# Optimization experiments

Hardware: AMD Instinct MI355X
Metric: run time of the kernel (lower is better)

Reference implementation:

```python
import jax, jax.numpy as jnp
import numpy as np
from jax import lax

D_MODEL = 1024
D_STATE = 16
D_CONV = 4
EXPAND = 2
D_INNER = EXPAND * D_MODEL  # 2048
DT_RANK = (D_MODEL + 15) // 16  # 64 (ceil(d_model/16), mamba default)
BATCH = 2
SEQLEN = 1024


def setup_inputs() -> dict:
    key = jax.random.key(0)
    ks = jax.random.split(key, 12)
    s = lambda k, shape, sc=0.02: jax.random.normal(k, shape, jnp.float32) * sc
    # A init: S4D-real, A_log = log(1..d_state) tiled over channels
    A_log = jnp.log(jnp.tile(jnp.arange(1, D_STATE + 1, dtype=jnp.float32), (D_INNER, 1)))
    # dt bias init so softplus(dt_bias) ~ 0.01
    dt_bias = jnp.log(jnp.expm1(jnp.full((D_INNER,), 0.01, jnp.float32)))
    return {
        "x": jax.random.normal(ks[0], (BATCH, SEQLEN, D_MODEL), jnp.float32),
        "in_proj_w": s(ks[1], (2 * D_INNER, D_MODEL)),
        "conv_w": s(ks[2], (D_INNER, 1, D_CONV), 0.1),
        "conv_b": s(ks[3], (D_INNER,), 0.1),
        "x_proj_w": s(ks[4], (DT_RANK + 2 * D_STATE, D_INNER)),
        "dt_proj_w": s(ks[5], (D_INNER, DT_RANK), 0.1),
        "dt_proj_b": dt_bias,
        "A_log": A_log,
        "D": jnp.ones((D_INNER,), jnp.float32),
        "out_proj_w": s(ks[6], (D_MODEL, D_INNER)),
        "ln1_g": jnp.ones((D_MODEL,), jnp.float32),
        "ln1_b": jnp.zeros((D_MODEL,), jnp.float32),
        "ln2_g": jnp.ones((D_MODEL,), jnp.float32),
        "ln2_b": jnp.zeros((D_MODEL,), jnp.float32),
        "ffn_w1": s(ks[7], (4 * D_MODEL, D_MODEL)),
        "ffn_b1": jnp.zeros((4 * D_MODEL,), jnp.float32),
        "ffn_w2": s(ks[8], (D_MODEL, 4 * D_MODEL)),
        "ffn_b2": jnp.zeros((D_MODEL,), jnp.float32),
    }


def _layernorm(x, g, b, eps=1e-5):
    mu = jnp.mean(x, axis=-1, keepdims=True)
    var = jnp.mean(jnp.square(x - mu), axis=-1, keepdims=True)
    return (x - mu) * lax.rsqrt(var + eps) * g + b


def _mamba(x, in_proj_w, conv_w, conv_b, x_proj_w, dt_proj_w, dt_proj_b,
           A_log, D, out_proj_w):
    Bsz, L, _ = x.shape
    xz = x @ in_proj_w.T                       # [B, L, 2*d_inner]
    xi, z = jnp.split(xz, 2, axis=-1)          # each [B, L, d_inner]
    # causal depthwise conv1d over time
    xc = xi.transpose(0, 2, 1)                 # [B, d_inner, L]
    xc = lax.conv_general_dilated(
        xc, conv_w, window_strides=(1,), padding=[(D_CONV - 1, 0)],
        feature_group_count=D_INNER,
        dimension_numbers=("NCH", "OIH", "NCH"))
    xc = xc + conv_b[None, :, None]
    xc = jax.nn.silu(xc).transpose(0, 2, 1)    # [B, L, d_inner]
    # input-dependent SSM params
    x_dbl = xc @ x_proj_w.T                    # [B, L, dt_rank + 2*d_state]
    dt, Bmat, Cmat = jnp.split(x_dbl, [DT_RANK, DT_RANK + D_STATE], axis=-1)
    dt = jax.nn.softplus(dt @ dt_proj_w.T + dt_proj_b)   # [B, L, d_inner]
    A = -jnp.exp(A_log)                        # [d_inner, d_state]
    dA = jnp.exp(dt[..., None] * A)                       # [B, L, d_inner, d_state]
    dBx = dt[..., None] * Bmat[:, :, None, :] * xc[..., None]  # [B, L, d_inner, d_state]
    # selective scan over time
    def step(h, inp):
        dA_t, dBx_t, C_t = inp
        h = dA_t * h + dBx_t                   # [B, d_inner, d_state]
        y = jnp.einsum("bdn,bn->bd", h, C_t)
        return h, y
    h0 = jnp.zeros((Bsz, D_INNER, D_STATE), x.dtype)
    _, ys = lax.scan(step, h0,
                     (dA.transpose(1, 0, 2, 3),
                      dBx.transpose(1, 0, 2, 3),
                      Cmat.transpose(1, 0, 2)))
    y = ys.transpose(1, 0, 2)                  # [B, L, d_inner]
    y = y + D * xc
    y = y * jax.nn.silu(z)
    return y @ out_proj_w.T                    # [B, L, d_model]


def reference(x, in_proj_w, conv_w, conv_b, x_proj_w, dt_proj_w, dt_proj_b,
              A_log, D, out_proj_w, ln1_g, ln1_b, ln2_g, ln2_b,
              ffn_w1, ffn_b1, ffn_w2, ffn_b2):
    # x = x + Mamba(LN1(x))
    x = x + _mamba(_layernorm(x, ln1_g, ln1_b), in_proj_w, conv_w, conv_b,
                   x_proj_w, dt_proj_w, dt_proj_b, A_log, D, out_proj_w)
    # x = x + FFN(LN2(x))  (dropout inactive in eval)
    h = _layernorm(x, ln2_g, ln2_b)
    f = jax.nn.relu(h @ ffn_w1.T + ffn_b1) @ ffn_w2.T + ffn_b2
    return x + f
```

## Files before the change

### kernel.cpp

```cpp
#include <hip/hip_runtime.h>
#include <hip/hip_bf16.h>

#define T_TOK 2048
#define LSEQ  1024
#define DM    1024
#define DI    2048
#define LDW2  72

using bf16 = __hip_bfloat16;
typedef __attribute__((ext_vector_type(8))) short short8;
typedef __attribute__((ext_vector_type(4))) short short4b;
typedef __attribute__((ext_vector_type(4))) float floatx4;

__device__ inline float to_f(float v) { return v; }
__device__ inline float to_f(bf16 v) { return __bfloat162float(v); }
__device__ inline bf16  f2bf(float v) { return __float2bfloat16(v); }
__device__ inline float bf2f(short s) { return __bfloat162float(__builtin_bit_cast(bf16, s)); }

__device__ inline short8 ld8(const bf16* p) { return *(const short8*)p; }
__device__ inline short8 ld8(const float* p) {
    floatx4 f0 = *(const floatx4*)p;
    floatx4 f1 = *(const floatx4*)(p + 4);
    short8 r;
#pragma unroll
    for (int i = 0; i < 4; ++i) {
        r[i]     = __builtin_bit_cast(short, __float2bfloat16(f0[i]));
        r[i + 4] = __builtin_bit_cast(short, __float2bfloat16(f1[i]));
    }
    return r;
}

__device__ __forceinline__ void gload16(const void* g, void* l) {
    __builtin_amdgcn_global_load_lds(
        (const __attribute__((address_space(1))) unsigned int*)g,
        (__attribute__((address_space(3))) unsigned int*)l, 16, 0, 0);
}

__device__ __forceinline__ int swz64(int row, int col) {
    return row * 64 + (col ^ ((row & 7) << 3));
}

template<int EPI, int KS>
__device__ __forceinline__ void gemm_core(
    const bf16* __restrict__ A, int lda,
    const bf16* __restrict__ W, int K,
    float* __restrict__ outF, bf16* __restrict__ outB, int ldc,
    const float* __restrict__ bias, size_t zstr)
{
    __shared__ __align__(16) bf16 sA[128 * 64];
    __shared__ __align__(16) bf16 sW[128 * 64];
    const int tid  = threadIdx.x;
    const int lane = tid & 63, wid = tid >> 6;

    const int nwg = gridDim.x * gridDim.y * gridDim.z;
    const int lin = blockIdx.x + gridDim.x * (blockIdx.y + gridDim.y * blockIdx.z);
    const int sid = (lin & 7) * (nwg >> 3) + (lin >> 3);
    const int bx  = sid % gridDim.x;
    const int byz = sid / gridDim.x;
    const int by  = byz % gridDim.y;
    const int bz  = byz / gridDim.y;

    const int m0 = bx * 128, n0 = by * 128;
    const int wm = (wid >> 2) * 64;
    const int wn = (wid & 3) * 32;
    const int lr = lane & 15, lh = lane >> 4;

    const int r0  = tid >> 3;
    const int gc0 = ((tid & 7) * 8) ^ ((r0 & 7) << 3);

    const int kBeg = bz * (K / KS);
    const int kEnd = kBeg + K / KS;

    const bf16* Ag0 = A + (size_t)(m0 + r0)      * lda + kBeg + gc0;
    const bf16* Ag1 = A + (size_t)(m0 + r0 + 64) * lda + kBeg + gc0;
    const bf16* Wg0 = W + (size_t)(n0 + r0)      * K   + kBeg + gc0;
    const bf16* Wg1 = W + (size_t)(n0 + r0 + 64) * K   + kBeg + gc0;

    bf16* sA0 = sA + wid * 512;
    bf16* sA1 = sA + 4096 + wid * 512;
    bf16* sW0 = sW + wid * 512;
    bf16* sW1 = sW + 4096 + wid * 512;

    floatx4 acc[4][2];
#pragma unroll
    for (int i = 0; i < 4; ++i)
#pragma unroll
        for (int j = 0; j < 2; ++j) acc[i][j] = (floatx4){0.f, 0.f, 0.f, 0.f};

    for (int k0 = kBeg; k0 < kEnd; k0 += 64) {
        __syncthreads();
        gload16(Ag0, sA0);
        gload16(Ag1, sA1);
        gload16(Wg0, sW0);
        gload16(Wg1, sW1);
        Ag0 += 64; Ag1 += 64; Wg0 += 64; Wg1 += 64;
        __syncthreads();

#pragma unroll
        for (int kk = 0; kk < 2; ++kk) {
            short8 af[4], wf[2];
#pragma unroll
            for (int i = 0; i < 4; ++i)
                af[i] = *(const short8*)(sA + swz64(wm + i * 16 + lr, kk * 32 + lh * 8));
#pragma unroll
            for (int j = 0; j < 2; ++j)
                wf[j] = *(const short8*)(sW + swz64(wn + j * 16 + lr, kk * 32 + lh * 8));
#pragma unroll
            for (int i = 0; i < 4; ++i)
#pragma unroll
                for (int j = 0; j < 2; ++j)
                    acc[i][j] = __builtin_amdgcn_mfma_f32_16x16x32_bf16(af[i], wf[j], acc[i][j], 0, 0, 0);
        }
    }

#pragma unroll
    for (int i = 0; i < 4; ++i) {
#pragma unroll
        for (int j = 0; j < 2; ++j) {
#pragma unroll
            for (int r = 0; r < 4; ++r) {
                int row = m0 + wm + i * 16 + lh * 4 + r;
                int col = n0 + wn + j * 16 + lr;
                size_t off = (size_t)row * ldc + col;
                float c = acc[i][j][r];
                if (EPI == 0) {
                    outB[off] = f2bf(c);
                } else if (EPI == 2) {
                    float v = c + bias[col];
                    outB[off] = f2bf((v > 15.f) ? v : log1pf(__expf(v)));
                } else if (EPI == 4) {
                    float v = c + bias[col];
                    outB[off] = f2bf(v > 0.f ? v : 0.f);
                } else if (EPI == 7) {
                    outF[off + (size_t)bz * zstr] = c;
                } else if (EPI == 8) {
                    outB[off + (size_t)bz * zstr] = f2bf(c);
                }
            }
        }
    }
}

__launch_bounds__(512, 4)
__global__ void g_inproj(const bf16* __restrict__ A, const bf16* __restrict__ W,
                         bf16* __restrict__ outB)
{ gemm_core<0, 1>(A, DM, W, DM, nullptr, outB, 4096, nullptr, 0); }

__launch_bounds__(512, 4)
__global__ void g_xproj(const bf16* __restrict__ A, const bf16* __restrict__ W,
                        float* __restrict__ outF)
{ gemm_core<7, 16>(A, DI, W, DI, outF, nullptr, 128, nullptr, (size_t)T_TOK * 128); }

__launch_bounds__(512, 4)
__global__ void g_outproj(const bf16* __restrict__ A, const bf16* __restrict__ W,
                          bf16* __restrict__ outB)
{ gemm_core<8, 4>(A, DI, W, DI, nullptr, outB, DM, nullptr, (size_t)T_TOK * DM); }

__launch_bounds__(512, 4)
__global__ void g_ffn1(const bf16* __restrict__ A, const bf16* __restrict__ W,
                       bf16* __restrict__ outB, const float* __restrict__ bias)
{ gemm_core<4, 1>(A, DM, W, DM, nullptr, outB, 4096, bias, 0); }

__launch_bounds__(512, 4)
__global__ void g_ffn2_4(const bf16* __restrict__ A, const bf16* __restrict__ W,
                         bf16* __restrict__ outB)
{ gemm_core<8, 4>(A, 4096, W, 4096, nullptr, outB, DM, nullptr, (size_t)T_TOK * DM); }

__launch_bounds__(512, 4)
__global__ void g_ffn2_2(const bf16* __restrict__ A, const bf16* __restrict__ W,
                         bf16* __restrict__ outB)
{ gemm_core<8, 2>(A, 4096, W, 4096, nullptr, outB, DM, nullptr, (size_t)T_TOK * DM); }

__launch_bounds__(256)
__global__ void cvtw(const float* __restrict__ src, bf16* __restrict__ dst)
{
    size_t i = ((size_t)blockIdx.x * 256 + threadIdx.x) * 8;
    *(short8*)(dst + i) = ld8(src + i);
}

__launch_bounds__(256)
__global__ void cvtw5(const float* __restrict__ s0, bf16* __restrict__ d0,
                      const float* __restrict__ s1, bf16* __restrict__ d1,
                      const float* __restrict__ s2, bf16* __restrict__ d2,
                      const float* __restrict__ s3, bf16* __restrict__ d3,
                      const float* __restrict__ s4, bf16* __restrict__ d4)
{
    constexpr size_t N0 = (size_t)2 * DI * DM;
    constexpr size_t N1 = (size_t)DM * DI;
    constexpr size_t N2 = (size_t)4 * DM * DM;
    constexpr size_t N3 = (size_t)DM * 4 * DM;
    size_t i = ((size_t)blockIdx.x * 256 + threadIdx.x) * 8;
    if (i < N0) { *(short8*)(d0 + i) = ld8(s0 + i); return; }
    i -= N0;
    if (i < N1) { *(short8*)(d1 + i) = ld8(s1 + i); return; }
    i -= N1;
    if (i < N2) { *(short8*)(d2 + i) = ld8(s2 + i); return; }
    i -= N2;
    if (i < N3) { *(short8*)(d3 + i) = ld8(s3 + i); return; }
    i -= N3;
    int row = (int)(i >> 11);
    if (row < 96) { *(short8*)(d4 + i) = ld8(s4 + i); }
    else { *(short8*)(d4 + i) = (short8){0,0,0,0,0,0,0,0}; }
}

__launch_bounds__(256)
__global__ void gemm_dt64(const float* __restrict__ A,
                          const float* __restrict__ W,
                          const float* __restrict__ bias,
                          bf16* __restrict__ outB)
{
    __shared__ __align__(16) bf16 sA[32 * LDW2];
    __shared__ __align__(16) bf16 sW[128 * LDW2];
    const int tid = threadIdx.x;
    const int lane = tid & 63, w = tid >> 6;
    const int m0 = blockIdx.x * 32, n0 = blockIdx.y * 128;

    {
        int ar = tid >> 3, ac = (tid & 7) * 8;
        *(short8*)(sA + ar * LDW2 + ac) = ld8(A + (size_t)(m0 + ar) * 128 + ac);
        int wr = tid >> 1, wc = (tid & 1) * 32;
        const float* wp = W + (size_t)(n0 + wr) * 64 + wc;
        *(short8*)(sW + wr * LDW2 + wc)      = ld8(wp);
        *(short8*)(sW + wr * LDW2 + wc + 8)  = ld8(wp + 8);
        *(short8*)(sW + wr * LDW2 + wc + 16) = ld8(wp + 16);
        *(short8*)(sW + wr * LDW2 + wc + 24) = ld8(wp + 24);
    }
    __syncthreads();

    const int lr = lane & 15, lh = lane >> 4;
    floatx4 acc[2][2];
#pragma unroll
    for (int i = 0; i < 2; ++i)
#pragma unroll
        for (int j = 0; j < 2; ++j) acc[i][j] = (floatx4){0.f, 0.f, 0.f, 0.f};

#pragma unroll
    for (int kk = 0; kk < 2; ++kk) {
        short8 af[2], wf[2];
#pragma unroll
        for (int i = 0; i < 2; ++i)
            af[i] = *(const short8*)(sA + (i * 16 + lr) * LDW2 + kk * 32 + lh * 8);
#pragma unroll
        for (int j = 0; j < 2; ++j)
            wf[j] = *(const short8*)(sW + (w * 32 + j * 16 + lr) * LDW2 + kk * 32 + lh * 8);
#pragma unroll
        for (int i = 0; i < 2; ++i)
#pragma unroll
            for (int j = 0; j < 2; ++j)
                acc[i][j] = __builtin_amdgcn_mfma_f32_16x16x32_bf16(af[i], wf[j], acc[i][j], 0, 0, 0);
    }

#pragma unroll
    for (int i = 0; i < 2; ++i) {
#pragma unroll
        for (int j = 0; j < 2; ++j) {
#pragma unroll
            for (int r = 0; r < 4; ++r) {
                int row = m0 + i * 16 + lh * 4 + r;
                int col = n0 + w * 32 + j * 16 + lr;
                float v = acc[i][j][r] + bias[col];
                outB[(size_t)row * DI + col] = f2bf((v > 15.f) ? v : log1pf(__expf(v)));
            }
        }
    }
}

__launch_bounds__(256)
__global__ void reduce16(const float* __restrict__ P, float* __restrict__ out)
{
    int i = blockIdx.x * 256 + threadIdx.x;
    const floatx4* P4 = (const floatx4*)P;
    floatx4 s = (floatx4){0.f, 0.f, 0.f, 0.f};
#pragma unroll
    for (int z = 0; z < 16; ++z) s += P4[(size_t)z * 65536 + i];
    ((floatx4*)out)[i] = s;
}

__launch_bounds__(256)
__global__ void red4_ln(const bf16* __restrict__ P, const float* __restrict__ x,
                        const float* __restrict__ g, const float* __restrict__ bb,
                        float* __restrict__ x2, bf16* __restrict__ h1)
{
    int t = blockIdx.x, tid = threadIdx.x;
    size_t rowoff = (size_t)t * DM + tid * 4;
    floatx4 xv = *(const floatx4*)(x + rowoff);
    float v[4];
#pragma unroll
    for (int i = 0; i < 4; ++i) v[i] = xv[i];
#pragma unroll
    for (int z = 0; z < 4; ++z) {
        short4b p = *(const short4b*)(P + (size_t)z * T_TOK * DM + rowoff);
#pragma unroll
        for (int i = 0; i < 4; ++i) v[i] += bf2f(p[i]);
    }
    *(floatx4*)(x2 + rowoff) = (floatx4){v[0], v[1], v[2], v[3]};
    float s = v[0] + v[1] + v[2] + v[3];
    float ss = v[0]*v[0] + v[1]*v[1] + v[2]*v[2] + v[3]*v[3];
#pragma unroll
    for (int o = 1; o < 64; o <<= 1) { s += __shfl_xor(s, o); ss += __shfl_xor(ss, o); }
    __shared__ float red[8];
    int lane = tid & 63, wid = tid >> 6;
    if (lane == 0) { red[wid] = s; red[wid + 4] = ss; }
    __syncthreads();
    s  = red[0] + red[1] + red[2] + red[3];
    ss = red[4] + red[5] + red[6] + red[7];
    float mu  = s * (1.f / DM);
    float var = ss * (1.f / DM) - mu * mu;
    float rs  = rsqrtf(var + 1e-5f);
    int c = tid * 4;
    short4b o4;
#pragma unroll
    for (int i = 0; i < 4; ++i)
        o4[i] = __builtin_bit_cast(short, f2bf((v[i] - mu) * rs * g[c + i] + bb[c + i]));
    *(short4b*)(h1 + rowoff) = o4;
}

template<int Z>
__launch_bounds__(256)
__global__ void red_bias_resid(const bf16* __restrict__ P, const float* __restrict__ bias,
                               const float* __restrict__ resid, float* __restrict__ out)
{
    size_t base = ((size_t)blockIdx.x * 256 + threadIdx.x) * 8;
    int c = (int)(base & (DM - 1));
    floatx4 b0 = *(const floatx4*)(bias + c);
    floatx4 b1 = *(const floatx4*)(bias + c + 4);
    floatx4 x0 = *(const floatx4*)(resid + base);
    floatx4 x1 = *(const floatx4*)(resid + base + 4);
    float s[8];
#pragma unroll
    for (int j = 0; j < 4; ++j) { s[j] = x0[j] + b0[j]; s[j + 4] = x1[j] + b1[j]; }
#pragma unroll
    for (int z = 0; z < Z; ++z) {
        short8 p = *(const short8*)(P + (size_t)z * T_TOK * DM + base);
#pragma unroll
        for (int j = 0; j < 8; ++j) s[j] += bf2f(p[j]);
    }
    *(floatx4*)(out + base)     = (floatx4){s[0], s[1], s[2], s[3]};
    *(floatx4*)(out + base + 4) = (floatx4){s[4], s[5], s[6], s[7]};
}

__launch_bounds__(256)
__global__ void ln_kernel(const float* __restrict__ x, const float* __restrict__ g,
                          const float* __restrict__ bb, bf16* __restrict__ out)
{
    int t = blockIdx.x, tid = threadIdx.x;
    const float* xr = x + (size_t)t * DM;
    float v[4], s = 0.f, ss = 0.f;
#pragma unroll
    for (int i = 0; i < 4; ++i) {
        v[i] = xr[tid + i * 256];
        s += v[i]; ss += v[i] * v[i];
    }
#pragma unroll
    for (int o = 1; o < 64; o <<= 1) { s += __shfl_xor(s, o); ss += __shfl_xor(ss, o); }
    __shared__ float red[8];
    int lane = tid & 63, wid = tid >> 6;
    if (lane == 0) { red[wid] = s; red[wid + 4] = ss; }
    __syncthreads();
    s  = red[0] + red[1] + red[2] + red[3];
    ss = red[4] + red[5] + red[6] + red[7];
    float mu  = s * (1.f / DM);
    float var = ss * (1.f / DM) - mu * mu;
    float rs  = rsqrtf(var + 1e-5f);
#pragma unroll
    for (int i = 0; i < 4; ++i) {
        int c = tid + i * 256;
        out[(size_t)t * DM + c] = f2bf((v[i] - mu) * rs * g[c] + bb[c]);
    }
}

__launch_bounds__(256)
__global__ void conv_silu(const bf16* __restrict__ xz, const float* __restrict__ cw,
                          const float* __restrict__ cb, bf16* __restrict__ xcb)
{
    int idx = (blockIdx.x * 256 + threadIdx.x) * 8;
    int d  = idx & (DI - 1);
    int tk = idx >> 11;
    int t  = tk & (LSEQ - 1);
    const short8 zero = {0, 0, 0, 0, 0, 0, 0, 0};
    short8 x3 = ld8(xz + (size_t)tk * 4096 + d);
    short8 x2 = (t >= 1) ? ld8(xz + (size_t)(tk - 1) * 4096 + d) : zero;
    short8 x1 = (t >= 2) ? ld8(xz + (size_t)(tk - 2) * 4096 + d) : zero;
    short8 x0 = (t >= 3) ? ld8(xz + (size_t)(tk - 3) * 4096 + d) : zero;
    short8 r;
#pragma unroll
    for (int j = 0; j < 8; ++j) {
        floatx4 wv = *(const floatx4*)(cw + (size_t)(d + j) * 4);
        float acc = cb[d + j]
                  + wv[0] * bf2f(x0[j]) + wv[1] * bf2f(x1[j])
                  + wv[2] * bf2f(x2[j]) + wv[3] * bf2f(x3[j]);
        float s = acc / (1.f + __expf(-acc));
        r[j] = __builtin_bit_cast(short, f2bf(s));
    }
    *(short8*)(xcb + idx) = r;
}

__launch_bounds__(256)
__global__ void padw_kernel(const float* __restrict__ w, bf16* __restrict__ wp)
{
    int idx = blockIdx.x * 256 + threadIdx.x;
    int row = idx >> 11;
    wp[idx] = (row < 96) ? f2bf(w[idx]) : f2bf(0.f);
}

template<int NCH_>
__launch_bounds__(256)
__global__ void scan_part1(const bf16* __restrict__ dt, const bf16* __restrict__ xc,
                           const float* __restrict__ xdbl, const float* __restrict__ A_log,
                           float* __restrict__ Ssum, float* __restrict__ hend)
{
    constexpr int CLEN_ = LSEQ / NCH_;
    constexpr int LOGN  = (NCH_ == 64) ? 6 : 5;
    int G = blockIdx.x * 256 + threadIdx.x;
    int half = G & 1;
    int d = (G >> 1) & (DI - 1);
    int c = (G >> 12) & (NCH_ - 1);
    int b = G >> (12 + LOGN);
    int n0 = half * 8;

    floatx4 al0 = *(const floatx4*)(A_log + d * 16 + n0);
    floatx4 al1 = *(const floatx4*)(A_log + d * 16 + n0 + 4);
    float a[8];
#pragma unroll
    for (int j = 0; j < 4; ++j) { a[j] = -__expf(al0[j]); a[j + 4] = -__expf(al1[j]); }

    const bf16*  dt_p = dt   + (size_t)b * LSEQ * DI + d;
    const bf16*  xc_p = xc   + (size_t)b * LSEQ * DI + d;
    const float* xb_p = xdbl + (size_t)b * LSEQ * 128 + 64 + n0;

    float h[8];
#pragma unroll
    for (int j = 0; j < 8; ++j) h[j] = 0.f;
    float S = 0.f;

    const int t0 = c * CLEN_;
#pragma unroll 4
    for (int t = t0; t < t0 + CLEN_; ++t) {
        float dtv = to_f(dt_p[(size_t)t * DI]);
        float xv  = to_f(xc_p[(size_t)t * DI]);
        floatx4 B0 = *(const floatx4*)(xb_p + (size_t)t * 128);
        floatx4 B1 = *(const floatx4*)(xb_p + (size_t)t * 128 + 4);
        S += dtv;
        float dx = dtv * xv;
#pragma unroll
        for (int j = 0; j < 4; ++j) {
            h[j]     = fmaf(__expf(dtv * a[j]),     h[j],     dx * B0[j]);
            h[j + 4] = fmaf(__expf(dtv * a[j + 4]), h[j + 4], dx * B1[j]);
        }
    }

    size_t cid = (size_t)(b * NCH_ + c) * DI + d;
    if (half == 0) Ssum[cid] = S;
    float* he = hend + cid * 16 + n0;
    *(floatx4*)he       = (floatx4){h[0], h[1], h[2], h[3]};
    *(floatx4*)(he + 4) = (floatx4){h[4], h[5], h[6], h[7]};
}

template<int NCH_>
__launch_bounds__(256)
__global__ void scan_prefix(const float* __restrict__ A_log, const float* __restrict__ Ssum,
                            float* __restrict__ hend)
{
    int tid = blockIdx.x * 256 + threadIdx.x;
    int n = tid & 15;
    int d = (tid >> 4) & (DI - 1);
    int b = tid >> 15;
    float a = -__expf(A_log[d * 16 + n]);

    size_t row = (size_t)b * NCH_ * DI + d;
    float Sc = Ssum[row];
    float E  = hend[row * 16 + n];
    float h = 0.f;
    for (int c = 0; c < NCH_; ++c) {
        size_t nrow = row + DI;
        float Sn = 0.f, En = 0.f;
        if (c + 1 < NCH_) { Sn = Ssum[nrow]; En = hend[nrow * 16 + n]; }
        float P = __expf(a * Sc);
        hend[row * 16 + n] = h;
        h  = fmaf(P, h, E);
        Sc = Sn; E = En; row = nrow;
    }
}

template<int NCH_>
__launch_bounds__(256)
__global__ void scan_part2(const bf16* __restrict__ dt, const bf16* __restrict__ xc,
                           const float* __restrict__ xdbl, const bf16* __restrict__ xz,
                           const float* __restrict__ hinit, const float* __restrict__ A_log,
                           const float* __restrict__ Dp, bf16* __restrict__ Y)
{
    constexpr int CLEN_ = LSEQ / NCH_;
    constexpr int LOGN  = (NCH_ == 64) ? 6 : 5;
    int G = blockIdx.x * 256 + threadIdx.x;
    int half = G & 1;
    int d = (G >> 1) & (DI - 1);
    int c = (G >> 12) & (NCH_ - 1);
    int b = G >> (12 + LOGN);
    int n0 = half * 8;

    floatx4 al0 = *(const floatx4*)(A_log + d * 16 + n0);
    floatx4 al1 = *(const floatx4*)(A_log + d * 16 + n0 + 4);
    float a[8];
#pragma unroll
    for (int j = 0; j < 4; ++j) { a[j] = -__expf(al0[j]); a[j + 4] = -__expf(al1[j]); }
    float Dd = Dp[d];

    size_t cid = (size_t)(b * NCH_ + c) * DI + d;
    const float* hi = hinit + cid * 16 + n0;
    floatx4 h0 = *(const floatx4*)hi;
    floatx4 h1 = *(const floatx4*)(hi + 4);
    float h[8] = {h0[0], h0[1], h0[2], h0[3], h1[0], h1[1], h1[2], h1[3]};

    const bf16*  dt_p = dt   + (size_t)b * LSEQ * DI + d;
    const bf16*  xc_p = xc   + (size_t)b * LSEQ * DI + d;
    const float* xb_p = xdbl + (size_t)b * LSEQ * 128 + 64 + n0;
    const float* xcc_p= xdbl + (size_t)b * LSEQ * 128 + 80 + n0;
    const bf16*  z_p  = xz   + (size_t)b * LSEQ * 4096 + DI + d;
    bf16* y_p = Y + (size_t)b * LSEQ * DI + d;

    const int t0 = c * CLEN_;
#pragma unroll 4
    for (int t = t0; t < t0 + CLEN_; ++t) {
        float dtv = to_f(dt_p[(size_t)t * DI]);
        float xv  = to_f(xc_p[(size_t)t * DI]);
        float zv  = to_f(z_p[(size_t)t * 4096]);
        floatx4 B0 = *(const floatx4*)(xb_p  + (size_t)t * 128);
        floatx4 B1 = *(const floatx4*)(xb_p  + (size_t)t * 128 + 4);
        floatx4 C0 = *(const floatx4*)(xcc_p + (size_t)t * 128);
        floatx4 C1 = *(const floatx4*)(xcc_p + (size_t)t * 128 + 4);
        float dx = dtv * xv;
        float p = 0.f;
#pragma unroll
        for (int j = 0; j < 4; ++j) {
            h[j]     = fmaf(__expf(dtv * a[j]),     h[j],     dx * B0[j]);
            p = fmaf(h[j], C0[j], p);
            h[j + 4] = fmaf(__expf(dtv * a[j + 4]), h[j + 4], dx * B1[j]);
            p = fmaf(h[j + 4], C1[j], p);
        }
        p += __shfl_xor(p, 1);
        if (half == 0) {
            float pp = p + Dd * xv;
            float sz = zv / (1.f + __expf(-zv));
            y_p[(size_t)t * DI] = f2bf(pp * sz);
        }
    }
}

extern "C" void kernel_launch(void* const* d_in, const int* in_sizes, int n_in,
                              void* d_out, int out_size, void* d_ws, size_t ws_size,
                              hipStream_t stream)
{
    const float* x       = (const float*)d_in[0];
    const float* in_proj = (const float*)d_in[1];
    const float* conv_w  = (const float*)d_in[2];
    const float* conv_b  = (const float*)d_in[3];
    const float* x_proj  = (const float*)d_in[4];
    const float* dt_w    = (const float*)d_in[5];
    const float* dt_b    = (const float*)d_in[6];
    const float* A_log   = (const float*)d_in[7];
    const float* Dp      = (const float*)d_in[8];
    const float* out_w   = (const float*)d_in[9];
    const float* ln1g    = (const float*)d_in[10];
    const float* ln1b    = (const float*)d_in[11];
    const float* ln2g    = (const float*)d_in[12];
    const float* ln2b    = (const float*)d_in[13];
    const float* fw1     = (const float*)d_in[14];
    const float* fb1     = (const float*)d_in[15];
    const float* fw2     = (const float*)d_in[16];
    const float* fb2     = (const float*)d_in[17];
    float* out = (float*)d_out;

    char* w = (char*)d_ws;
    bf16*  h1   = (bf16*)(w);
    bf16*  xz   = (bf16*)(w + (4u  << 20));
    bf16*  xc   = (bf16*)(w + (20u << 20));
    float* xdf  = (float*)(w + (28u << 20));
    bf16*  dtb  = (bf16*)(w + (29u << 20));
    float* Pp   = (float*)(w + (29u << 20));
    float* hend = (float*)(w + (37u << 20));
    float* x2   = (float*)(w + (37u << 20));
    bf16*  Wpad = (bf16*)(w + (45u << 20));
    float* Ssum = (float*)(w);
    bf16*  Pout = (bf16*)(w + (4u  << 20));
    bf16*  Yb = xc;
    bf16*  f1 = xz;

    const bool roomy = ws_size >= ((size_t)74 << 20);

    if (roomy) {
        bf16* ipB  = (bf16*)(w + (46u << 20));
        bf16* owB  = (bf16*)(w + (54u << 20));
        bf16* fw1B = (bf16*)(w + (58u << 20));
        bf16* fw2B = (bf16*)(w + (66u << 20));
        bf16* Pf   = (bf16*)(w + (20u << 20));

        cvtw5<<<dim3(7296), dim3(256), 0, stream>>>(in_proj, ipB, out_w, owB,
                                                    fw1, fw1B, fw2, fw2B, x_proj, Wpad);
        ln_kernel<<<dim3(T_TOK), dim3(256), 0, stream>>>(x, ln1g, ln1b, h1);
        g_inproj<<<dim3(16, 32), dim3(512), 0, stream>>>(h1, ipB, xz);
        conv_silu<<<dim3(T_TOK * DI / 8 / 256), dim3(256), 0, stream>>>(xz, conv_w, conv_b, xc);
        g_xproj<<<dim3(16, 1, 16), dim3(512), 0, stream>>>(xc, Wpad, Pp);
        reduce16<<<dim3(256), dim3(256), 0, stream>>>(Pp, xdf);
        gemm_dt64<<<dim3(64, 16), dim3(256), 0, stream>>>(xdf, dt_w, dt_b, dtb);
        scan_part1<64><<<dim3(2048), dim3(256), 0, stream>>>(dtb, xc, xdf, A_log, Ssum, hend);
        scan_prefix<64><<<dim3(256), dim3(256), 0, stream>>>(A_log, Ssum, hend);
        scan_part2<64><<<dim3(2048), dim3(256), 0, stream>>>(dtb, xc, xdf, xz, hend, A_log, Dp, Yb);
        g_outproj<<<dim3(16, 8, 4), dim3(512), 0, stream>>>(Yb, owB, Pout);
        red4_ln<<<dim3(T_TOK), dim3(256), 0, stream>>>(Pout, x, ln2g, ln2b, x2, h1);
        g_ffn1<<<dim3(16, 32), dim3(512), 0, stream>>>(h1, fw1B, f1, fb1);
        g_ffn2_4<<<dim3(16, 8, 4), dim3(512), 0, stream>>>(f1, fw2B, Pf);
        red_bias_resid<4><<<dim3(1024), dim3(256), 0, stream>>>(Pf, fb2, x2, out);
    } else {
        bf16* ipB  = (bf16*)(w + (20u << 20));
        bf16* owB  = (bf16*)(w);
        bf16* fw1B = (bf16*)(w + (29u << 20));
        bf16* fw2B = (bf16*)(w + (20u << 20));
        bf16* Pf   = (bf16*)(w + (28u << 20));

        cvtw<<<dim3(2048), dim3(256), 0, stream>>>(in_proj, ipB);
        ln_kernel<<<dim3(T_TOK), dim3(256), 0, stream>>>(x, ln1g, ln1b, h1);
        g_inproj<<<dim3(16, 32), dim3(512), 0, stream>>>(h1, ipB, xz);
        conv_silu<<<dim3(T_TOK * DI / 8 / 256), dim3(256), 0, stream>>>(xz, conv_w, conv_b, xc);
        padw_kernel<<<dim3(128 * 2048 / 256), dim3(256), 0, stream>>>(x_proj, Wpad);
        g_xproj<<<dim3(16, 1, 16), dim3(512), 0, stream>>>(xc, Wpad, Pp);
        reduce16<<<dim3(256), dim3(256), 0, stream>>>(Pp, xdf);
        gemm_dt64<<<dim3(64, 16), dim3(256), 0, stream>>>(xdf, dt_w, dt_b, dtb);
        scan_part1<32><<<dim3(1024), dim3(256), 0, stream>>>(dtb, xc, xdf, A_log, Ssum, hend);
        scan_prefix<32><<<dim3(256), dim3(256), 0, stream>>>(A_log, Ssum, hend);
        cvtw<<<dim3(1024), dim3(256), 0, stream>>>(out_w, owB);
        scan_part2<32><<<dim3(1024), dim3(256), 0, stream>>>(dtb, xc, xdf, xz, hend, A_log, Dp, Yb);
        g_outproj<<<dim3(16, 8, 4), dim3(512), 0, stream>>>(Yb, owB, Pout);
        cvtw<<<dim3(2048), dim3(256), 0, stream>>>(fw1, fw1B);
        red4_ln<<<dim3(T_TOK), dim3(256), 0, stream>>>(Pout, x, ln2g, ln2b, x2, h1);
        g_ffn1<<<dim3(16, 32), dim3(512), 0, stream>>>(h1, fw1B, f1, fb1);
        cvtw<<<dim3(2048), dim3(256), 0, stream>>>(fw2, fw2B);
        g_ffn2_2<<<dim3(16, 8, 2), dim3(512), 0, stream>>>(f1, fw2B, Pf);
        red_bias_resid<2><<<dim3(1024), dim3(256), 0, stream>>>(Pf, fb2, x2, out);
    }
}
```

Baseline: 340.0 us.

## Double-buffer GEMM LDS tiles and fuse LN1 into weight conversion kernel

The shared GEMM core now keeps two LDS buffers per operand and issues the global-to-LDS loads for the next K tile before running the MFMAs on the current one. This is meant to overlap memory latency with compute, at the cost of doubling LDS use to 64KB per block, which may lower occupancy. Separately, the first LayerNorm is merged into the weight-conversion kernel as extra blocks, removing one launch. The fused LN computes variance as E[x^2]-mu^2, which is slightly less numerically stable. The loop steps K by 128 and relies on each K slice being a multiple of 128.

```diff
diff --git a/kernel.cpp b/kernel.cpp
--- a/kernel.cpp
+++ b/kernel.cpp
@@ -47,8 +47,8 @@
     float* __restrict__ outF, bf16* __restrict__ outB, int ldc,
     const float* __restrict__ bias, size_t zstr)
 {
-    __shared__ __align__(16) bf16 sA[128 * 64];
-    __shared__ __align__(16) bf16 sW[128 * 64];
+    __shared__ __align__(16) bf16 sA[2 * 128 * 64];
+    __shared__ __align__(16) bf16 sW[2 * 128 * 64];
     const int tid  = threadIdx.x;
     const int lane = tid & 63, wid = tid >> 6;
 
@@ -76,42 +76,55 @@
     const bf16* Wg0 = W + (size_t)(n0 + r0)      * K   + kBeg + gc0;
     const bf16* Wg1 = W + (size_t)(n0 + r0 + 64) * K   + kBeg + gc0;
 
-    bf16* sA0 = sA + wid * 512;
-    bf16* sA1 = sA + 4096 + wid * 512;
-    bf16* sW0 = sW + wid * 512;
-    bf16* sW1 = sW + 4096 + wid * 512;
-
     floatx4 acc[4][2];
 #pragma unroll
     for (int i = 0; i < 4; ++i)
 #pragma unroll
         for (int j = 0; j < 2; ++j) acc[i][j] = (floatx4){0.f, 0.f, 0.f, 0.f};
 
-    for (int k0 = kBeg; k0 < kEnd; k0 += 64) {
+#define STAGE(B, KOFF) do {                                           \
+        gload16(Ag0 + (KOFF), sA + (B) * 8192 + wid * 512);           \
+        gload16(Ag1 + (KOFF), sA + (B) * 8192 + 4096 + wid * 512);    \
+        gload16(Wg0 + (KOFF), sW + (B) * 8192 + wid * 512);           \
+        gload16(Wg1 + (KOFF), sW + (B) * 8192 + 4096 + wid * 512);    \
+    } while (0)
+
+#define COMPUTE(B) do {                                                        \
+        const bf16* bA = sA + (B) * 8192;                                      \
+        const bf16* bW = sW + (B) * 8192;                                      \
+        _Pragma("unroll")                                                      \
+        for (int kk = 0; kk < 2; ++kk) {                                       \
+            short8 af[4], wf[2];                                               \
+            _Pragma("unroll")                                                  \
+            for (int i = 0; i < 4; ++i)                                        \
+                af[i] = *(const short8*)(bA + swz64(wm + i * 16 + lr,          \
+                                                    kk * 32 + lh * 8));        \
+            _Pragma("unroll")                                                  \
+            for (int j = 0; j < 2; ++j)                                        \
+                wf[j] = *(const short8*)(bW + swz64(wn + j * 16 + lr,          \
+                                                    kk * 32 + lh * 8));        \
+            _Pragma("unroll")                                                  \
+            for (int i = 0; i < 4; ++i)                                        \
+                _Pragma("unroll")                                              \
+                for (int j = 0; j < 2; ++j)                                    \
+                    acc[i][j] = __builtin_amdgcn_mfma_f32_16x16x32_bf16(       \
+                        af[i], wf[j], acc[i][j], 0, 0, 0);                     \
+        }                                                                      \
+    } while (0)
+
+    STAGE(0, 0);
+    __syncthreads();
+    for (int k0 = kBeg; k0 < kEnd; k0 += 128) {
+        int koff = k0 - kBeg;
+        if (k0 + 64 < kEnd) STAGE(1, koff + 64);
+        COMPUTE(0);
         __syncthreads();
-        gload16(Ag0, sA0);
-        gload16(Ag1, sA1);
-        gload16(Wg0, sW0);
-        gload16(Wg1, sW1);
-        Ag0 += 64; Ag1 += 64; Wg0 += 64; Wg1 += 64;
+        if (k0 + 128 < kEnd) STAGE(0, koff + 128);
+        COMPUTE(1);
         __syncthreads();
-
-#pragma unroll
-        for (int kk = 0; kk < 2; ++kk) {
-            short8 af[4], wf[2];
-#pragma unroll
-            for (int i = 0; i < 4; ++i)
-                af[i] = *(const short8*)(sA + swz64(wm + i * 16 + lr, kk * 32 + lh * 8));
-#pragma unroll
-            for (int j = 0; j < 2; ++j)
-                wf[j] = *(const short8*)(sW + swz64(wn + j * 16 + lr, kk * 32 + lh * 8));
-#pragma unroll
-            for (int i = 0; i < 4; ++i)
-#pragma unroll
-                for (int j = 0; j < 2; ++j)
-                    acc[i][j] = __builtin_amdgcn_mfma_f32_16x16x32_bf16(af[i], wf[j], acc[i][j], 0, 0, 0);
-        }
-    }
+    }
+#undef STAGE
+#undef COMPUTE
 
 #pragma unroll
     for (int i = 0; i < 4; ++i) {
@@ -179,17 +192,46 @@
 }
 
 __launch_bounds__(256)
-__global__ void cvtw5(const float* __restrict__ s0, bf16* __restrict__ d0,
-                      const float* __restrict__ s1, bf16* __restrict__ d1,
-                      const float* __restrict__ s2, bf16* __restrict__ d2,
-                      const float* __restrict__ s3, bf16* __restrict__ d3,
-                      const float* __restrict__ s4, bf16* __restrict__ d4)
-{
+__global__ void pre_ln_cvt(const float* __restrict__ x, const float* __restrict__ g,
+                           const float* __restrict__ bb, bf16* __restrict__ h1,
+                           const float* __restrict__ s0, bf16* __restrict__ d0,
+                           const float* __restrict__ s1, bf16* __restrict__ d1,
+                           const float* __restrict__ s2, bf16* __restrict__ d2,
+                           const float* __restrict__ s3, bf16* __restrict__ d3,
+                           const float* __restrict__ s4, bf16* __restrict__ d4)
+{
+    int blk = blockIdx.x, tid = threadIdx.x;
+    if (blk < T_TOK) {
+        const float* xr = x + (size_t)blk * DM;
+        float v[4], s = 0.f, ss = 0.f;
+#pragma unroll
+        for (int i = 0; i < 4; ++i) {
+            v[i] = xr[tid + i * 256];
+            s += v[i]; ss += v[i] * v[i];
+        }
+#pragma unroll
+        for (int o = 1; o < 64; o <<= 1) { s += __shfl_xor(s, o); ss += __shfl_xor(ss, o); }
+        __shared__ float red[8];
+        int lane = tid & 63, wid = tid >> 6;
+        if (lane == 0) { red[wid] = s; red[wid + 4] = ss; }
+        __syncthreads();
+        s  = red[0] + red[1] + red[2] + red[3];
+        ss = red[4] + red[5] + red[6] + red[7];
+        float mu  = s * (1.f / DM);
+        float var = ss * (1.f / DM) - mu * mu;
+        float rs  = rsqrtf(var + 1e-5f);
+#pragma unroll
+        for (int i = 0; i < 4; ++i) {
+            int c = tid + i * 256;
+            h1[(size_t)blk * DM + c] = f2bf((v[i] - mu) * rs * g[c] + bb[c]);
+        }
+        return;
+    }
     constexpr size_t N0 = (size_t)2 * DI * DM;
     constexpr size_t N1 = (size_t)DM * DI;
     constexpr size_t N2 = (size_t)4 * DM * DM;
     constexpr size_t N3 = (size_t)DM * 4 * DM;
-    size_t i = ((size_t)blockIdx.x * 256 + threadIdx.x) * 8;
+    size_t i = ((size_t)(blk - T_TOK) * 256 + tid) * 8;
     if (i < N0) { *(short8*)(d0 + i) = ld8(s0 + i); return; }
     i -= N0;
     if (i < N1) { *(short8*)(d1 + i) = ld8(s1 + i); return; }
@@ -594,9 +636,9 @@
         bf16* fw2B = (bf16*)(w + (66u << 20));
         bf16* Pf   = (bf16*)(w + (20u << 20));
 
-        cvtw5<<<dim3(7296), dim3(256), 0, stream>>>(in_proj, ipB, out_w, owB,
-                                                    fw1, fw1B, fw2, fw2B, x_proj, Wpad);
-        ln_kernel<<<dim3(T_TOK), dim3(256), 0, stream>>>(x, ln1g, ln1b, h1);
+        pre_ln_cvt<<<dim3(T_TOK + 7296), dim3(256), 0, stream>>>(
+            x, ln1g, ln1b, h1,
+            in_proj, ipB, out_w, owB, fw1, fw1B, fw2, fw2B, x_proj, Wpad);
         g_inproj<<<dim3(16, 32), dim3(512), 0, stream>>>(h1, ipB, xz);
         conv_silu<<<dim3(T_TOK * DI / 8 / 256), dim3(256), 0, stream>>>(xz, conv_w, conv_b, xc);
         g_xproj<<<dim3(16, 1, 16), dim3(512), 0, stream>>>(xc, Wpad, Pp);
```

Result: no change. 334.0 us (-1.8%).
